# Optimization experiments

Hardware: AMD Instinct MI355X
Metric: run time of the kernel (lower is better)

The kernel has to match this reference:

```python
import jax, jax.numpy as jnp
import numpy as np

BF = 2          # branching_factor
NH = 8          # num_heads
DIM = 64        # dim
PAD = BF + 1    # padding value in path words
N_POS = 2048    # number of positions precomputed


def _pos_to_path(idx, cache):
    if idx in cache:
        return cache[idx]
    parent = (idx - 2) // BF + 1 if idx != 1 else -1
    step = (idx - 2) % BF + 1 if idx != 1 else 0
    cache[idx] = [*_pos_to_path(parent, cache), step]
    return cache[idx]


def setup_inputs() -> dict:
    key = jax.random.key(0)
    # raw parameter: torch.rand -> uniform [0,1)
    primitives_raw = jax.random.uniform(key, (BF * NH + 1, DIM, DIM), dtype=jnp.float32)
    cache = {1: [], 0: [-1], -1: []}
    paths = [_pos_to_path(p, cache) for p in range(N_POS)]
    max_len = max(len(p) for p in paths)
    pw = np.full((N_POS, max_len), PAD, dtype=np.int32)
    for i, p in enumerate(paths):
        pw[i, :len(p)] = p
    return {"primitives_raw": primitives_raw, "path_words": jnp.asarray(pw)}


def reference(primitives_raw, path_words):
    dim = primitives_raw.shape[-1]
    # primitives = expm((A - A^H) / dim); real-valued so mH == transpose
    herm = (primitives_raw - jnp.swapaxes(primitives_raw, -1, -2)) / dim
    prims = jax.vmap(jax.scipy.linalg.expm)(herm)          # [BF*NH+1, d, d]
    sos_repr = prims[-1]                                   # [d, d]
    branch = prims[:-1].reshape(BF, NH, dim, dim)          # [BF, NH, d, d]

    # ---- steps (integer, no grad in original) ----
    point_mask = path_words != PAD                         # [N, L]
    pair_mask = point_mask[:, None, :] & point_mask[None, :, :]
    eqs = (path_words[:, None, :] == path_words[None, :, :]).astype(jnp.int32)
    common_prefix = jnp.cumprod(eqs, axis=-1).astype(bool) & pair_mask
    lens = point_mask.sum(-1)
    max_lens = jnp.maximum(lens[:, None], lens[None, :])
    steps = max_lens - common_prefix.sum(-1)               # [N, N]

    # ---- maps: sequential product of primitives along each path ----
    n = path_words.shape[0]
    eye = jnp.eye(dim, dtype=prims.dtype)
    init = jnp.broadcast_to(eye, (n, NH, dim, dim))
    sos = path_words[:, 0] == -1
    init = jnp.where(sos[:, None, None, None], sos_repr[None, None], init)

    def body(maps, idx_t):
        # Faithful to source: only k in range(BF) matches (value BF acts as identity)
        gate = (idx_t >= 0) & (idx_t < BF)                 # [N]
        mats = jnp.where(gate[:, None, None, None],
                         branch[jnp.clip(idx_t, 0, BF - 1)],  # [N, NH, d, d]
                         eye)
        return jnp.einsum('nhij,nhjk->nhik', maps, mats), None

    maps, _ = jax.lax.scan(body, init, path_words.T)       # scan over depth L
    return maps, steps
```

## Files before the change

kernel.cpp:

```cpp
#include <hip/hip_runtime.h>

#define DIM 64
#define NHEADS 8
#define NPOS 2048
#define PADW 3

typedef float f32x4 __attribute__((ext_vector_type(4)));

#define C1 1.0f
#define C2 0.5f
#define C3 (1.0f / 6.0f)
#define C4 (1.0f / 24.0f)
#define C5 (1.0f / 120.0f)
#define C6 (1.0f / 720.0f)
#define C7 (1.0f / 5040.0f)
#define C8 (1.0f / 40320.0f)

__device__ __forceinline__ f32x4 ld4(const float* p) { return *reinterpret_cast<const f32x4*>(p); }
__device__ __forceinline__ void st4(float* p, f32x4 v) { *reinterpret_cast<f32x4*>(p) = v; }
__device__ __forceinline__ void tzero(float (&a)[4][4]) {
#pragma unroll
  for (int i = 0; i < 4; ++i)
#pragma unroll
    for (int j = 0; j < 4; ++j) a[i][j] = 0.0f;
}
__device__ __forceinline__ void tfma(float (&a)[4][4], const f32x4 x, const f32x4 y) {
#pragma unroll
  for (int i = 0; i < 4; ++i)
#pragma unroll
    for (int j = 0; j < 4; ++j) a[i][j] = fmaf(x[i], y[j], a[i][j]);
}

__global__ __launch_bounds__(256, 1) void prologue_kernel(const float* __restrict__ U,
                                                          float* __restrict__ powers) {
  __shared__ __align__(16) float b0[4096];
  __shared__ __align__(16) float b1[4096];
  __shared__ __align__(16) float b2[4096];
  __shared__ __align__(16) float b3[4096];
  const int t = threadIdx.x;
  const int b = blockIdx.x;
  const bool sos = (b == 88);
  const int kp = sos ? 1 : (b >> 3);
  float* __restrict__ dst = powers + (size_t)b * 4096;

  if (kp == 0) {
    for (int i = t; i < 4096; i += 256) dst[i] = ((i >> 6) == (i & 63)) ? 1.0f : 0.0f;
    return;
  }

  const int m = sos ? 16 : (NHEADS + (b & 7));
  const float* __restrict__ Um = U + (size_t)m * 4096;
  const float scale = (float)kp * (1.0f / 256.0f);

  const int r0 = ((t >> 4) & 15) << 2;
  const int c0 = (t & 15) << 2;

  {
    f32x4 ur[4], uc[4];
#pragma unroll
    for (int i = 0; i < 4; ++i) ur[i] = ld4(&Um[(r0 + i) * 64 + c0]);
#pragma unroll
    for (int j = 0; j < 4; ++j) uc[j] = ld4(&Um[(c0 + j) * 64 + r0]);
#pragma unroll
    for (int i = 0; i < 4; ++i) {
      f32x4 v;
#pragma unroll
      for (int j = 0; j < 4; ++j) v[j] = scale * (ur[i][j] - uc[j][i]);
      st4(&b0[(r0 + i) * 64 + c0], v);
    }
  }
  __syncthreads();

  {
    float a[4][4];
    tzero(a);
#pragma unroll 4
    for (int k = 0; k < 64; ++k) tfma(a, ld4(&b0[k * 64 + r0]), ld4(&b0[k * 64 + c0]));
#pragma unroll
    for (int i = 0; i < 4; ++i) {
      f32x4 v;
#pragma unroll
      for (int j = 0; j < 4; ++j) v[j] = -a[i][j];
      st4(&b1[(r0 + i) * 64 + c0], v);
    }
  }
  __syncthreads();

  {
    float a3[4][4], a4[4][4];
    tzero(a3);
    tzero(a4);
#pragma unroll 4
    for (int k = 0; k < 64; ++k) {
      const f32x4 msr = ld4(&b0[k * 64 + r0]);
      const f32x4 m2r = ld4(&b1[k * 64 + r0]);
      const f32x4 m2c = ld4(&b1[k * 64 + c0]);
      tfma(a3, msr, m2c);
      tfma(a4, m2r, m2c);
    }
#pragma unroll
    for (int i = 0; i < 4; ++i) {
      f32x4 v3, v4;
#pragma unroll
      for (int j = 0; j < 4; ++j) {
        v3[j] = -a3[i][j];
        v4[j] = a4[i][j];
      }
      st4(&b2[(r0 + i) * 64 + c0], v3);
      st4(&b3[(r0 + i) * 64 + c0], v4);
    }
  }
  __syncthreads();

  {
    float aE[4][4], aO[4][4];
    tzero(aE);
    tzero(aO);
#pragma unroll 2
    for (int k = 0; k < 64; ++k) {
      const f32x4 xv = ld4(&b3[k * 64 + r0]);
      const f32x4 msv = ld4(&b0[k * 64 + c0]);
      const f32x4 m2v = ld4(&b1[k * 64 + c0]);
      const f32x4 m3v = ld4(&b2[k * 64 + c0]);
      const f32x4 m4v = ld4(&b3[k * 64 + c0]);
      f32x4 ev, ov, yv, yw;
#pragma unroll
      for (int j = 0; j < 4; ++j) {
        ev[j] = fmaf(C8, m4v[j], C6 * m2v[j]);
        ov[j] = fmaf(C7, m3v[j], C5 * msv[j]);
        yv[j] = ev[j] + ov[j];
        yw[j] = ev[j] - ov[j];
      }
      tfma(aE, xv, yv);
      tfma(aO, xv, yw);
    }
    float eT[4][4], oT[4][4];
#pragma unroll
    for (int i = 0; i < 4; ++i) {
      const f32x4 msr = ld4(&b0[(r0 + i) * 64 + c0]);
      const f32x4 m2r = ld4(&b1[(r0 + i) * 64 + c0]);
      const f32x4 m3r = ld4(&b2[(r0 + i) * 64 + c0]);
      const f32x4 m4r = ld4(&b3[(r0 + i) * 64 + c0]);
#pragma unroll
      for (int j = 0; j < 4; ++j) {
        const float d = (r0 + i == c0 + j) ? 1.0f : 0.0f;
        const float even = d + fmaf(C4, m4r[j], C2 * m2r[j]);
        const float odd = fmaf(C3, m3r[j], C1 * msr[j]);
        eT[i][j] = aE[i][j] + even + odd;
        oT[i][j] = aO[i][j] + even - odd;
      }
    }
    __syncthreads();
#pragma unroll
    for (int i = 0; i < 4; ++i) {
      f32x4 ve, vo;
#pragma unroll
      for (int j = 0; j < 4; ++j) {
        ve[j] = eT[i][j];
        vo[j] = oT[i][j];
      }
      st4(&b0[(r0 + i) * 64 + c0], ve);
      st4(&b1[(r0 + i) * 64 + c0], vo);
    }
  }
  __syncthreads();

  {
    float aA[4][4], aB[4][4];
    tzero(aA);
    tzero(aB);
#pragma unroll 2
    for (int k = 0; k < 64; ++k) {
      const f32x4 etr = ld4(&b1[k * 64 + r0]);
      const f32x4 er = ld4(&b0[k * 64 + r0]);
      const f32x4 ec = ld4(&b0[k * 64 + c0]);
      const f32x4 etc2 = ld4(&b1[k * 64 + c0]);
      tfma(aA, etr, ec);
      tfma(aB, er, etc2);
    }
#pragma unroll
    for (int i = 0; i < 4; ++i) {
      f32x4 va, vb;
#pragma unroll
      for (int j = 0; j < 4; ++j) {
        va[j] = aA[i][j];
        vb[j] = aB[i][j];
      }
      st4(&b2[(r0 + i) * 64 + c0], va);
      st4(&b3[(r0 + i) * 64 + c0], vb);
    }
  }
  __syncthreads();

  {
    float a[4][4];
    tzero(a);
#pragma unroll 4
    for (int k = 0; k < 64; ++k) tfma(a, ld4(&b3[k * 64 + r0]), ld4(&b2[k * 64 + c0]));
#pragma unroll
    for (int i = 0; i < 4; ++i) {
      f32x4 v;
#pragma unroll
      for (int j = 0; j < 4; ++j) v[j] = a[i][j];
      st4(&dst[(r0 + i) * 64 + c0], v);
    }
  }
}

__global__ __launch_bounds__(256) void outputs_kernel(const float* __restrict__ powers,
                                                      const int* __restrict__ pw, int L,
                                                      float* __restrict__ out_maps,
                                                      float* __restrict__ out_steps) {
  const int t = threadIdx.x;
  if (blockIdx.x < 64 * 64) {
    const int tb = blockIdx.x;
    const int bi = (tb >> 6) * 32, bj = (tb & 63) * 32;
    __shared__ unsigned long long pki[32], pkj[32];
    __shared__ int li[32], lj[32];
    if (t < 64) {
      const int r = (t < 32) ? (bi + t) : (bj + (t - 32));
      const int* row = pw + (size_t)r * L;
      int len = 0;
      unsigned long long packed = 0ull;
      for (int s = 0; s < L; ++s) {
        const int w = row[s];
        len += (w != PADW) ? 1 : 0;
        packed |= (unsigned long long)(unsigned)(w + 1) << (3 * s);
      }
      if (t < 32) {
        pki[t] = packed;
        li[t] = len;
      } else {
        pkj[t - 32] = packed;
        lj[t - 32] = len;
      }
    }
    __syncthreads();
    const int tx = t & 31, ty0 = t >> 5;
    const unsigned long long xj = pkj[tx];
    const int lenj = lj[tx];
#pragma unroll
    for (int m = 0; m < 4; ++m) {
      const int ty = ty0 + 8 * m;
      const unsigned long long x = pki[ty] ^ xj;
      const int leni = li[ty];
      const int p = x ? (__builtin_ctzll(x) / 3) : L;
      const int common = min(p, min(leni, lenj));
      const float steps = (float)(max(leni, lenj) - common);
      out_steps[(size_t)(bi + ty) * NPOS + (bj + tx)] = steps;
    }
  } else {
    const int n = blockIdx.x - 64 * 64;
    const int* row = pw + (size_t)n * L;
    const bool sos = (row[0] == -1);
    int c = 0;
    for (int s = 0; s < L; ++s) {
      const int w = row[s];
      c += (w >= 0 && w < 2) ? 1 : 0;
    }
#pragma unroll
    for (int h = 0; h < NHEADS; ++h) {
      const float* src = sos ? (powers + (size_t)88 * 4096)
                             : (powers + (size_t)(c * NHEADS + h) * 4096);
      const f32x4* s4 = reinterpret_cast<const f32x4*>(src);
      f32x4* d4 = reinterpret_cast<f32x4*>(out_maps + ((size_t)n * NHEADS + h) * 4096);
#pragma unroll
      for (int i = 0; i < 4; ++i) d4[t + 256 * i] = s4[t + 256 * i];
    }
  }
}

extern "C" void kernel_launch(void* const* d_in, const int* in_sizes, int n_in,
                              void* d_out, int out_size, void* d_ws, size_t ws_size,
                              hipStream_t stream) {
  const float* U = (const float*)d_in[0];
  const int* pw = (const int*)d_in[1];
  const int L = in_sizes[1] / NPOS;

  float* powers = (float*)d_ws;

  float* out_maps = (float*)d_out;
  float* out_steps = out_maps + (size_t)NPOS * NHEADS * 4096;

  hipLaunchKernelGGL(prologue_kernel, dim3(89), dim3(256), 0, stream, U, powers);
  hipLaunchKernelGGL(outputs_kernel, dim3(64 * 64 + NPOS), dim3(256), 0, stream,
                     powers, pw, L, out_maps, out_steps);
}
```

Measured before the change: 298.2 us.

## Move steps computation into prologue kernel and use nontemporal stores

The pairwise steps blocks now run in the first kernel alongside the 89 matrix-exponential blocks instead of the second kernel. This lets the steps output writes overlap the serial prologue compute rather than waiting behind it. Both output paths now use nontemporal stores to avoid polluting cache with write-only data. The risk is that steps blocks inherit the prologue's 64KB shared memory allocation and launch bound of 1, which lowers their occupancy.

```diff
diff --git a/kernel.cpp b/kernel.cpp
--- a/kernel.cpp
+++ b/kernel.cpp
@@ -31,14 +31,59 @@
     for (int j = 0; j < 4; ++j) a[i][j] = fmaf(x[i], y[j], a[i][j]);
 }
 
-__global__ __launch_bounds__(256, 1) void prologue_kernel(const float* __restrict__ U,
-                                                          float* __restrict__ powers) {
+__global__ __launch_bounds__(256, 1) void pre_kernel(const float* __restrict__ U,
+                                                     float* __restrict__ powers,
+                                                     const int* __restrict__ pw, int L,
+                                                     float* __restrict__ out_steps) {
   __shared__ __align__(16) float b0[4096];
   __shared__ __align__(16) float b1[4096];
   __shared__ __align__(16) float b2[4096];
   __shared__ __align__(16) float b3[4096];
   const int t = threadIdx.x;
   const int b = blockIdx.x;
+
+  if (b >= 89) {
+    const int tb = b - 89;
+    const int bi = (tb >> 6) * 32, bj = (tb & 63) * 32;
+    unsigned long long* pki = reinterpret_cast<unsigned long long*>(b0);
+    unsigned long long* pkj = pki + 32;
+    int* li = reinterpret_cast<int*>(pkj + 32);
+    int* lj = li + 32;
+    if (t < 64) {
+      const int r = (t < 32) ? (bi + t) : (bj + (t - 32));
+      const int* row = pw + (size_t)r * L;
+      int len = 0;
+      unsigned long long packed = 0ull;
+      for (int s = 0; s < L; ++s) {
+        const int w = row[s];
+        len += (w != PADW) ? 1 : 0;
+        packed |= (unsigned long long)(unsigned)(w + 1) << (3 * s);
+      }
+      if (t < 32) {
+        pki[t] = packed;
+        li[t] = len;
+      } else {
+        pkj[t - 32] = packed;
+        lj[t - 32] = len;
+      }
+    }
+    __syncthreads();
+    const int tx = t & 31, ty0 = t >> 5;
+    const unsigned long long xj = pkj[tx];
+    const int lenj = lj[tx];
+#pragma unroll
+    for (int m = 0; m < 4; ++m) {
+      const int ty = ty0 + 8 * m;
+      const unsigned long long x = pki[ty] ^ xj;
+      const int leni = li[ty];
+      const int p = x ? (__builtin_ctzll(x) / 3) : L;
+      const int common = min(p, min(leni, lenj));
+      const float steps = (float)(max(leni, lenj) - common);
+      __builtin_nontemporal_store(steps, &out_steps[(size_t)(bi + ty) * NPOS + (bj + tx)]);
+    }
+    return;
+  }
+
   const bool sos = (b == 88);
   const int kp = sos ? 1 : (b >> 3);
   float* __restrict__ dst = powers + (size_t)b * 4096;
@@ -207,65 +252,28 @@
   }
 }
 
-__global__ __launch_bounds__(256) void outputs_kernel(const float* __restrict__ powers,
-                                                      const int* __restrict__ pw, int L,
-                                                      float* __restrict__ out_maps,
-                                                      float* __restrict__ out_steps) {
+__global__ __launch_bounds__(256) void maps_kernel(const float* __restrict__ powers,
+                                                   const int* __restrict__ pw, int L,
+                                                   float* __restrict__ out_maps) {
   const int t = threadIdx.x;
-  if (blockIdx.x < 64 * 64) {
-    const int tb = blockIdx.x;
-    const int bi = (tb >> 6) * 32, bj = (tb & 63) * 32;
-    __shared__ unsigned long long pki[32], pkj[32];
-    __shared__ int li[32], lj[32];
-    if (t < 64) {
-      const int r = (t < 32) ? (bi + t) : (bj + (t - 32));
-      const int* row = pw + (size_t)r * L;
-      int len = 0;
-      unsigned long long packed = 0ull;
-      for (int s = 0; s < L; ++s) {
-        const int w = row[s];
-        len += (w != PADW) ? 1 : 0;
-        packed |= (unsigned long long)(unsigned)(w + 1) << (3 * s);
-      }
-      if (t < 32) {
-        pki[t] = packed;
-        li[t] = len;
-      } else {
-        pkj[t - 32] = packed;
-        lj[t - 32] = len;
-      }
-    }
-    __syncthreads();
-    const int tx = t & 31, ty0 = t >> 5;
-    const unsigned long long xj = pkj[tx];
-    const int lenj = lj[tx];
-#pragma unroll
-    for (int m = 0; m < 4; ++m) {
-      const int ty = ty0 + 8 * m;
-      const unsigned long long x = pki[ty] ^ xj;
-      const int leni = li[ty];
-      const int p = x ? (__builtin_ctzll(x) / 3) : L;
-      const int common = min(p, min(leni, lenj));
-      const float steps = (float)(max(leni, lenj) - common);
-      out_steps[(size_t)(bi + ty) * NPOS + (bj + tx)] = steps;
-    }
-  } else {
-    const int n = blockIdx.x - 64 * 64;
-    const int* row = pw + (size_t)n * L;
-    const bool sos = (row[0] == -1);
-    int c = 0;
-    for (int s = 0; s < L; ++s) {
-      const int w = row[s];
-      c += (w >= 0 && w < 2) ? 1 : 0;
-    }
-#pragma unroll
-    for (int h = 0; h < NHEADS; ++h) {
-      const float* src = sos ? (powers + (size_t)88 * 4096)
-                             : (powers + (size_t)(c * NHEADS + h) * 4096);
-      const f32x4* s4 = reinterpret_cast<const f32x4*>(src);
-      f32x4* d4 = reinterpret_cast<f32x4*>(out_maps + ((size_t)n * NHEADS + h) * 4096);
-#pragma unroll
-      for (int i = 0; i < 4; ++i) d4[t + 256 * i] = s4[t + 256 * i];
+  const int n = blockIdx.x;
+  const int* row = pw + (size_t)n * L;
+  const bool sos = (row[0] == -1);
+  int c = 0;
+  for (int s = 0; s < L; ++s) {
+    const int w = row[s];
+    c += (w >= 0 && w < 2) ? 1 : 0;
+  }
+#pragma unroll
+  for (int h = 0; h < NHEADS; ++h) {
+    const float* src = sos ? (powers + (size_t)88 * 4096)
+                           : (powers + (size_t)(c * NHEADS + h) * 4096);
+    const f32x4* s4 = reinterpret_cast<const f32x4*>(src);
+    f32x4* d4 = reinterpret_cast<f32x4*>(out_maps + ((size_t)n * NHEADS + h) * 4096);
+#pragma unroll
+    for (int i = 0; i < 4; ++i) {
+      const f32x4 v = s4[t + 256 * i];
+      __builtin_nontemporal_store(v, &d4[t + 256 * i]);
     }
   }
 }
@@ -282,7 +290,8 @@
   float* out_maps = (float*)d_out;
   float* out_steps = out_maps + (size_t)NPOS * NHEADS * 4096;
 
-  hipLaunchKernelGGL(prologue_kernel, dim3(89), dim3(256), 0, stream, U, powers);
-  hipLaunchKernelGGL(outputs_kernel, dim3(64 * 64 + NPOS), dim3(256), 0, stream,
-                     powers, pw, L, out_maps, out_steps);
-}
+  hipLaunchKernelGGL(pre_kernel, dim3(89 + 64 * 64), dim3(256), 0, stream, U, powers,
+                     pw, L, out_steps);
+  hipLaunchKernelGGL(maps_kernel, dim3(NPOS), dim3(256), 0, stream, powers, pw, L,
+                     out_maps);
+}
```

After: 302.4 us. No clear change (+1.4%).
